# Kernel tuning notes

Hardware: AMD Instinct MI355X
Metric: run time of the kernel (lower is better)

Reference implementation:

```python
import jax, jax.numpy as jnp
import numpy as np

TAU = 18.0


def smooth_compose(X, M, tau=TAU):
    # Z[n,i,j] = smooth_min(X[n,i], M[i,j]) = -(1/tau) * log(exp(-tau*X) + exp(-tau*M))
    # Y[n,j]   = (1/tau) * logsumexp(tau * Z[n,:,j], axis over i)
    # tau*Z = -logaddexp(-tau*X, -tau*M)  (numerically stable, same math)
    tZ = -jnp.logaddexp(-tau * X[:, :, None], -tau * M[None, :, :])  # [n, d, d]
    return (1.0 / tau) * jax.nn.logsumexp(tZ, axis=1)  # [n, d]


def setup_inputs() -> dict:
    key = jax.random.key(0)
    k1, k2, k3, k4, k5 = jax.random.split(key, 5)
    n, p, d = 2048, 1024, 256
    S = jax.random.uniform(k1, (n, p), dtype=jnp.float32)
    T = jax.random.uniform(k2, (n, p), dtype=jnp.float32)
    # learned parameters (A0/M0/B0 defaults are 0.5-filled; use random values of similar scale)
    A = jax.random.uniform(k3, (p, d), dtype=jnp.float32)
    # rawM = logit(M0); random small logits -> M = sigmoid(rawM) near 0.5
    rawM = 0.5 * jax.random.normal(k4, (d, d), dtype=jnp.float32)
    B = jax.random.uniform(k5, (d, p), dtype=jnp.float32)
    return {"S": S, "T": T, "A": A, "rawM": rawM, "B": B}


def reference(S, T, A, rawM, B):
    M = jax.nn.sigmoid(rawM)            # [d, d]
    X_hat = S @ A                       # [n, d]
    Y_hat = T @ A                       # [n, d]
    X_box = jnp.clip(X_hat, 0.0, 1.0)
    Y_box = jnp.clip(Y_hat, 0.0, 1.0)
    Y_pred = smooth_compose(X_box, M, tau=TAU)  # [n, d]
    S_rec = X_hat @ B                   # [n, p]
    T_rec = Y_hat @ B                   # [n, p]
    T_pred = Y_pred @ B                 # [n, p]
    return (X_hat, Y_hat, X_box, Y_box, Y_pred, S_rec, T_rec, T_pred)
```

## Files before the change

kernel.cpp:

```cpp
#include <hip/hip_runtime.h>
#include <math.h>

constexpr int N = 2048;
constexpr int P = 1024;
constexpr int D = 256;
constexpr float TAU = 18.0f;

constexpr size_t OFF_XHAT  = 0;
constexpr size_t OFF_YHAT  = (size_t)N * D;
constexpr size_t OFF_XBOX  = 2 * (size_t)N * D;
constexpr size_t OFF_YBOX  = 3 * (size_t)N * D;
constexpr size_t OFF_YPRED = 4 * (size_t)N * D;
constexpr size_t OFF_SREC  = 5 * (size_t)N * D;

constexpr size_t WS_ATH = 0;
constexpr size_t WS_ATL = 524288;
constexpr size_t WS_BTH = 1048576;
constexpr size_t WS_BTL = 1572864;
constexpr size_t WS_V   = 2097152;
constexpr size_t WS_U   = 2359296;

typedef short bhalf8 __attribute__((ext_vector_type(8)));
typedef float f32x4  __attribute__((ext_vector_type(4)));

__device__ inline short f2bf(float f) {
  union { float f; unsigned u; } x; x.f = f;
  unsigned r = (x.u + 0x7FFFu + ((x.u >> 16) & 1u)) >> 16;
  return (short)r;
}
__device__ inline float bf2f(short h) {
  union { unsigned u; float f; } x; x.u = ((unsigned)(unsigned short)h) << 16;
  return x.f;
}

__global__ __launch_bounds__(256) void prep_v_kernel(
    const float* __restrict__ rawM, float* __restrict__ V) {
  const int idx = (blockIdx.x * 256 + threadIdx.x) * 4;
  float4 x = *(const float4*)(rawM + idx);
  float4 o;
  o.x = expf(-TAU / (1.0f + expf(-x.x)));
  o.y = expf(-TAU / (1.0f + expf(-x.y)));
  o.z = expf(-TAU / (1.0f + expf(-x.z)));
  o.w = expf(-TAU / (1.0f + expf(-x.w)));
  *(float4*)(V + idx) = o;
}

__global__ __launch_bounds__(256) void transpose_hilo_kernel(
    const float* __restrict__ src, short* __restrict__ dh,
    short* __restrict__ dl, int R, int C) {
  __shared__ __align__(16) float tile[32][36];
  const int t = threadIdx.x;
  const int r0 = blockIdx.x * 32, c0 = blockIdx.y * 32;
  {
    const int tr = t >> 3, tc4 = (t & 7) * 4;
    float4 x = *(const float4*)(src + (size_t)(r0 + tr) * C + c0 + tc4);
    *(float4*)&tile[tr][tc4] = x;
  }
  __syncthreads();
  {
    const int tc = t >> 3, tr4 = (t & 7) * 4;
    short4 h, l;
    float f0 = tile[tr4 + 0][tc];
    float f1 = tile[tr4 + 1][tc];
    float f2 = tile[tr4 + 2][tc];
    float f3 = tile[tr4 + 3][tc];
    h.x = f2bf(f0); l.x = f2bf(f0 - bf2f(h.x));
    h.y = f2bf(f1); l.y = f2bf(f1 - bf2f(h.y));
    h.z = f2bf(f2); l.z = f2bf(f2 - bf2f(h.z));
    h.w = f2bf(f3); l.w = f2bf(f3 - bf2f(h.w));
    *(short4*)(dh + (size_t)(c0 + tc) * R + r0 + tr4) = h;
    *(short4*)(dl + (size_t)(c0 + tc) * R + r0 + tr4) = l;
  }
}

__global__ __launch_bounds__(256) void gemm1_mfma(
    const float* __restrict__ S, const float* __restrict__ Tm,
    const short* __restrict__ Ath, const short* __restrict__ Atl,
    float* __restrict__ out, float* __restrict__ U) {
  __shared__ __align__(16) short As_h[64][40];
  __shared__ __align__(16) short As_l[64][40];
  __shared__ __align__(16) short Bs_h[64][40];
  __shared__ __align__(16) short Bs_l[64][40];

  const int t = threadIdx.x;
  const int m0 = blockIdx.x * 64, n0 = blockIdx.y * 64;

  const int arow = t >> 2;
  const int koct = (t & 3) * 8;
  const int grow = m0 + arow;
  const float* Lrow = (grow < N) ? (S + (size_t)grow * P)
                                 : (Tm + (size_t)(grow - N) * P);
  const short* Bh_row = Ath + (size_t)(n0 + arow) * P;
  const short* Bl_row = Atl + (size_t)(n0 + arow) * P;

  const int l = t & 63, w = t >> 6;
  const int wr = (w >> 1) * 32, wc = (w & 1) * 32;
  const int fr = l & 15;
  const int ko = (l >> 4) * 8;
  const int rq = (l >> 4) * 4;

  f32x4 acc[2][2];
#pragma unroll
  for (int i = 0; i < 2; ++i)
#pragma unroll
    for (int j = 0; j < 2; ++j) acc[i][j] = (f32x4){0.f, 0.f, 0.f, 0.f};

  float4 a0 = *(const float4*)(Lrow + koct);
  float4 a1 = *(const float4*)(Lrow + koct + 4);
  bhalf8 bh = *(const bhalf8*)(Bh_row + koct);
  bhalf8 bl = *(const bhalf8*)(Bl_row + koct);

  for (int ks = 0; ks < P / 32; ++ks) {
    __syncthreads();
    {
      float af[8] = {a0.x, a0.y, a0.z, a0.w, a1.x, a1.y, a1.z, a1.w};
      bhalf8 ah, al;
#pragma unroll
      for (int q = 0; q < 8; ++q) {
        short h = f2bf(af[q]);
        ah[q] = h;
        al[q] = f2bf(af[q] - bf2f(h));
      }
      *(bhalf8*)&As_h[arow][koct] = ah;
      *(bhalf8*)&As_l[arow][koct] = al;
      *(bhalf8*)&Bs_h[arow][koct] = bh;
      *(bhalf8*)&Bs_l[arow][koct] = bl;
    }
    __syncthreads();
    if (ks + 1 < P / 32) {
      const int kn = (ks + 1) * 32 + koct;
      a0 = *(const float4*)(Lrow + kn);
      a1 = *(const float4*)(Lrow + kn + 4);
      bh = *(const bhalf8*)(Bh_row + kn);
      bl = *(const bhalf8*)(Bl_row + kn);
    }
    bhalf8 avh[2], avl[2], bvh[2], bvl[2];
#pragma unroll
    for (int mi = 0; mi < 2; ++mi) {
      avh[mi] = *(const bhalf8*)&As_h[wr + mi * 16 + fr][ko];
      avl[mi] = *(const bhalf8*)&As_l[wr + mi * 16 + fr][ko];
      bvh[mi] = *(const bhalf8*)&Bs_h[wc + mi * 16 + fr][ko];
      bvl[mi] = *(const bhalf8*)&Bs_l[wc + mi * 16 + fr][ko];
    }
#pragma unroll
    for (int mi = 0; mi < 2; ++mi)
#pragma unroll
      for (int ni = 0; ni < 2; ++ni) {
        acc[mi][ni] = __builtin_amdgcn_mfma_f32_16x16x32_bf16(avh[mi], bvh[ni], acc[mi][ni], 0, 0, 0);
        acc[mi][ni] = __builtin_amdgcn_mfma_f32_16x16x32_bf16(avh[mi], bvl[ni], acc[mi][ni], 0, 0, 0);
        acc[mi][ni] = __builtin_amdgcn_mfma_f32_16x16x32_bf16(avl[mi], bvh[ni], acc[mi][ni], 0, 0, 0);
        acc[mi][ni] = __builtin_amdgcn_mfma_f32_16x16x32_bf16(avl[mi], bvl[ni], acc[mi][ni], 0, 0, 0);
      }
  }

#pragma unroll
  for (int mi = 0; mi < 2; ++mi)
#pragma unroll
    for (int ni = 0; ni < 2; ++ni) {
      const int col = n0 + wc + ni * 16 + fr;
#pragma unroll
      for (int r = 0; r < 4; ++r) {
        const int row = m0 + wr + mi * 16 + rq + r;
        const float v = acc[mi][ni][r];
        const float c = fminf(fmaxf(v, 0.0f), 1.0f);
        if (row < N) {
          out[OFF_XHAT + (size_t)row * D + col] = v;
          out[OFF_XBOX + (size_t)row * D + col] = c;
          U[(size_t)row * D + col] = expf(-TAU * c);
        } else {
          const size_t ry = (size_t)(row - N);
          out[OFF_YHAT + ry * D + col] = v;
          out[OFF_YBOX + ry * D + col] = c;
        }
      }
    }
}

__global__ __launch_bounds__(256) void smooth_kernel(
    const float* __restrict__ U, const float* __restrict__ V,
    float* __restrict__ ypred) {
  __shared__ float us[256][33];
  const int t = threadIdx.x;
  const int n0 = blockIdx.x * 32, j0 = blockIdx.y * 64;

  {
    const int sr = t & 31;
    const int si = (t >> 5) * 32;
    const float* up = U + (size_t)(n0 + sr) * D + si;
#pragma unroll
    for (int q = 0; q < 32; q += 4) {
      float4 x = *(const float4*)(up + q);
      us[si + q + 0][sr] = x.x;
      us[si + q + 1][sr] = x.y;
      us[si + q + 2][sr] = x.z;
      us[si + q + 3][sr] = x.w;
    }
  }
  __syncthreads();

  const int jg = (t & 15) * 4;
  const int nn = (t >> 4) * 2;
  const float* vp = V + j0 + jg;

  float acc[2][4] = {};
#pragma unroll 4
  for (int i = 0; i < D; ++i) {
    const float u0 = us[i][nn];
    const float u1 = us[i][nn + 1];
    float4 v4 = *(const float4*)(vp + (size_t)i * D);
    acc[0][0] += __builtin_amdgcn_rcpf(u0 + v4.x);
    acc[0][1] += __builtin_amdgcn_rcpf(u0 + v4.y);
    acc[0][2] += __builtin_amdgcn_rcpf(u0 + v4.z);
    acc[0][3] += __builtin_amdgcn_rcpf(u0 + v4.w);
    acc[1][0] += __builtin_amdgcn_rcpf(u1 + v4.x);
    acc[1][1] += __builtin_amdgcn_rcpf(u1 + v4.y);
    acc[1][2] += __builtin_amdgcn_rcpf(u1 + v4.z);
    acc[1][3] += __builtin_amdgcn_rcpf(u1 + v4.w);
  }
#pragma unroll
  for (int pI = 0; pI < 2; ++pI) {
    float4 o;
    o.x = (1.0f / TAU) * logf(acc[pI][0]);
    o.y = (1.0f / TAU) * logf(acc[pI][1]);
    o.z = (1.0f / TAU) * logf(acc[pI][2]);
    o.w = (1.0f / TAU) * logf(acc[pI][3]);
    *(float4*)(ypred + (size_t)(n0 + nn + pI) * D + j0 + jg) = o;
  }
}

__global__ __launch_bounds__(256) void gemm2_mfma(
    const float* __restrict__ dout, const short* __restrict__ Bth,
    const short* __restrict__ Btl, float* __restrict__ rec) {
  __shared__ __align__(16) short As_h[64][40];
  __shared__ __align__(16) short As_l[64][40];
  __shared__ __align__(16) short Bs_h[64][40];
  __shared__ __align__(16) short Bs_l[64][40];

  const int t = threadIdx.x;
  const int m0 = blockIdx.x * 64, n0 = blockIdx.y * 64;

  const int arow = t >> 2;
  const int koct = (t & 3) * 8;
  const int grow = m0 + arow;
  const float* Lrow = (grow < 2 * N)
                          ? (dout + (size_t)grow * D)
                          : (dout + OFF_YPRED + (size_t)(grow - 2 * N) * D);
  const short* Bh_row = Bth + (size_t)(n0 + arow) * D;
  const short* Bl_row = Btl + (size_t)(n0 + arow) * D;

  const int l = t & 63, w = t >> 6;
  const int wr = (w >> 1) * 32, wc = (w & 1) * 32;
  const int fr = l & 15;
  const int ko = (l >> 4) * 8;
  const int rq = (l >> 4) * 4;

  f32x4 acc[2][2];
#pragma unroll
  for (int i = 0; i < 2; ++i)
#pragma unroll
    for (int j = 0; j < 2; ++j) acc[i][j] = (f32x4){0.f, 0.f, 0.f, 0.f};

  float4 a0 = *(const float4*)(Lrow + koct);
  float4 a1 = *(const float4*)(Lrow + koct + 4);
  bhalf8 bh = *(const bhalf8*)(Bh_row + koct);
  bhalf8 bl = *(const bhalf8*)(Bl_row + koct);

  for (int ks = 0; ks < D / 32; ++ks) {
    __syncthreads();
    {
      float af[8] = {a0.x, a0.y, a0.z, a0.w, a1.x, a1.y, a1.z, a1.w};
      bhalf8 ah, al;
#pragma unroll
      for (int q = 0; q < 8; ++q) {
        short h = f2bf(af[q]);
        ah[q] = h;
        al[q] = f2bf(af[q] - bf2f(h));
      }
      *(bhalf8*)&As_h[arow][koct] = ah;
      *(bhalf8*)&As_l[arow][koct] = al;
      *(bhalf8*)&Bs_h[arow][koct] = bh;
      *(bhalf8*)&Bs_l[arow][koct] = bl;
    }
    __syncthreads();
    if (ks + 1 < D / 32) {
      const int kn = (ks + 1) * 32 + koct;
      a0 = *(const float4*)(Lrow + kn);
      a1 = *(const float4*)(Lrow + kn + 4);
      bh = *(const bhalf8*)(Bh_row + kn);
      bl = *(const bhalf8*)(Bl_row + kn);
    }
    bhalf8 avh[2], avl[2], bvh[2], bvl[2];
#pragma unroll
    for (int mi = 0; mi < 2; ++mi) {
      avh[mi] = *(const bhalf8*)&As_h[wr + mi * 16 + fr][ko];
      avl[mi] = *(const bhalf8*)&As_l[wr + mi * 16 + fr][ko];
      bvh[mi] = *(const bhalf8*)&Bs_h[wc + mi * 16 + fr][ko];
      bvl[mi] = *(const bhalf8*)&Bs_l[wc + mi * 16 + fr][ko];
    }
#pragma unroll
    for (int mi = 0; mi < 2; ++mi)
#pragma unroll
      for (int ni = 0; ni < 2; ++ni) {
        acc[mi][ni] = __builtin_amdgcn_mfma_f32_16x16x32_bf16(avh[mi], bvh[ni], acc[mi][ni], 0, 0, 0);
        acc[mi][ni] = __builtin_amdgcn_mfma_f32_16x16x32_bf16(avh[mi], bvl[ni], acc[mi][ni], 0, 0, 0);
        acc[mi][ni] = __builtin_amdgcn_mfma_f32_16x16x32_bf16(avl[mi], bvh[ni], acc[mi][ni], 0, 0, 0);
        acc[mi][ni] = __builtin_amdgcn_mfma_f32_16x16x32_bf16(avl[mi], bvl[ni], acc[mi][ni], 0, 0, 0);
      }
  }

#pragma unroll
  for (int mi = 0; mi < 2; ++mi)
#pragma unroll
    for (int ni = 0; ni < 2; ++ni) {
      const int col = n0 + wc + ni * 16 + fr;
#pragma unroll
      for (int r = 0; r < 4; ++r) {
        const int row = m0 + wr + mi * 16 + rq + r;
        rec[(size_t)row * P + col] = acc[mi][ni][r];
      }
    }
}

extern "C" void kernel_launch(void* const* d_in, const int* in_sizes, int n_in,
                              void* d_out, int out_size, void* d_ws,
                              size_t ws_size, hipStream_t stream) {
  const float* S    = (const float*)d_in[0];
  const float* T    = (const float*)d_in[1];
  const float* A    = (const float*)d_in[2];
  const float* rawM = (const float*)d_in[3];
  const float* B    = (const float*)d_in[4];
  float* out = (float*)d_out;
  char* ws = (char*)d_ws;

  short* Ath = (short*)(ws + WS_ATH);
  short* Atl = (short*)(ws + WS_ATL);
  short* Bth = (short*)(ws + WS_BTH);
  short* Btl = (short*)(ws + WS_BTL);
  float* V   = (float*)(ws + WS_V);
  float* U   = (float*)(ws + WS_U);

  prep_v_kernel<<<64, 256, 0, stream>>>(rawM, V);
  transpose_hilo_kernel<<<dim3(32, 8), 256, 0, stream>>>(A, Ath, Atl, P, D);
  transpose_hilo_kernel<<<dim3(8, 32), 256, 0, stream>>>(B, Bth, Btl, D, P);
  gemm1_mfma<<<dim3(64, 4), 256, 0, stream>>>(S, T, Ath, Atl, out, U);
  smooth_kernel<<<dim3(64, 4), 256, 0, stream>>>(U, V, out + OFF_YPRED);
  gemm2_mfma<<<dim3(96, 16), 256, 0, stream>>>(out, Bth, Btl, out + OFF_SREC);
}
```

Measured before the change: 158.7 us.

## Double-buffer GEMM tiles, drop lo*lo MFMA, pre-split GEMM2 operands to bf16

Both MFMA GEMMs move to 512-thread blocks with double-buffered LDS tiles and one barrier per k-step. The lo*lo bf16 correction product is dropped, removing a quarter of the MFMAs at a small precision cost. GEMM1 and the smooth kernel now write hi/lo bf16 splits of their outputs to workspace, so GEMM2 loads pre-split shorts instead of converting fp32 activations on each tile. The smooth kernel gets a smaller column tile to launch more blocks. The cost is extra workspace traffic for the split buffers.

```diff
diff --git a/kernel.cpp b/kernel.cpp
--- a/kernel.cpp
+++ b/kernel.cpp
@@ -19,6 +19,8 @@
 constexpr size_t WS_BTL = 1572864;
 constexpr size_t WS_V   = 2097152;
 constexpr size_t WS_U   = 2359296;
+constexpr size_t WS_LHH = 4456448;
+constexpr size_t WS_LHL = 7602176;
 
 typedef short bhalf8 __attribute__((ext_vector_type(8)));
 typedef float f32x4  __attribute__((ext_vector_type(4)));
@@ -73,115 +75,109 @@
   }
 }
 
-__global__ __launch_bounds__(256) void gemm1_mfma(
+__global__ __launch_bounds__(512) void gemm1_mfma(
     const float* __restrict__ S, const float* __restrict__ Tm,
     const short* __restrict__ Ath, const short* __restrict__ Atl,
-    float* __restrict__ out, float* __restrict__ U) {
-  __shared__ __align__(16) short As_h[64][40];
-  __shared__ __align__(16) short As_l[64][40];
-  __shared__ __align__(16) short Bs_h[64][40];
-  __shared__ __align__(16) short Bs_l[64][40];
-
-  const int t = threadIdx.x;
+    float* __restrict__ out, float* __restrict__ U,
+    short* __restrict__ LHh, short* __restrict__ LHl) {
+  __shared__ __align__(16) short As_h[2][64][40];
+  __shared__ __align__(16) short As_l[2][64][40];
+  __shared__ __align__(16) short Bs_h[2][64][40];
+  __shared__ __align__(16) short Bs_l[2][64][40];
+
+  const int t  = threadIdx.x;
   const int m0 = blockIdx.x * 64, n0 = blockIdx.y * 64;
 
-  const int arow = t >> 2;
-  const int koct = (t & 3) * 8;
-  const int grow = m0 + arow;
+  const int srow = t >> 3;
+  const int sk   = (t & 7) * 4;
+  const int grow = m0 + srow;
   const float* Lrow = (grow < N) ? (S + (size_t)grow * P)
                                  : (Tm + (size_t)(grow - N) * P);
-  const short* Bh_row = Ath + (size_t)(n0 + arow) * P;
-  const short* Bl_row = Atl + (size_t)(n0 + arow) * P;
+  const short* BhR = Ath + (size_t)(n0 + srow) * P;
+  const short* BlR = Atl + (size_t)(n0 + srow) * P;
 
   const int l = t & 63, w = t >> 6;
-  const int wr = (w >> 1) * 32, wc = (w & 1) * 32;
-  const int fr = l & 15;
-  const int ko = (l >> 4) * 8;
-  const int rq = (l >> 4) * 4;
-
-  f32x4 acc[2][2];
-#pragma unroll
-  for (int i = 0; i < 2; ++i)
-#pragma unroll
-    for (int j = 0; j < 2; ++j) acc[i][j] = (f32x4){0.f, 0.f, 0.f, 0.f};
-
-  float4 a0 = *(const float4*)(Lrow + koct);
-  float4 a1 = *(const float4*)(Lrow + koct + 4);
-  bhalf8 bh = *(const bhalf8*)(Bh_row + koct);
-  bhalf8 bl = *(const bhalf8*)(Bl_row + koct);
-
-  for (int ks = 0; ks < P / 32; ++ks) {
+  const int wr = (w & 3) * 16, wc = (w >> 2) * 32;
+  const int fr = l & 15, ko8 = (l >> 4) * 8, rq = (l >> 4) * 4;
+
+  f32x4 acc[2];
+  acc[0] = (f32x4){0.f, 0.f, 0.f, 0.f};
+  acc[1] = (f32x4){0.f, 0.f, 0.f, 0.f};
+
+  float4 pa  = *(const float4*)(Lrow + sk);
+  short4 pbh = *(const short4*)(BhR + sk);
+  short4 pbl = *(const short4*)(BlR + sk);
+
+#define STAGE1(buf)                                        \
+  do {                                                     \
+    short4 ah4, al4;                                       \
+    ah4.x = f2bf(pa.x); al4.x = f2bf(pa.x - bf2f(ah4.x));  \
+    ah4.y = f2bf(pa.y); al4.y = f2bf(pa.y - bf2f(ah4.y));  \
+    ah4.z = f2bf(pa.z); al4.z = f2bf(pa.z - bf2f(ah4.z));  \
+    ah4.w = f2bf(pa.w); al4.w = f2bf(pa.w - bf2f(ah4.w));  \
+    *(short4*)&As_h[buf][srow][sk] = ah4;                  \
+    *(short4*)&As_l[buf][srow][sk] = al4;                  \
+    *(short4*)&Bs_h[buf][srow][sk] = pbh;                  \
+    *(short4*)&Bs_l[buf][srow][sk] = pbl;                  \
+  } while (0)
+
+  STAGE1(0);
+
+  for (int ks = 0; ks < 32; ++ks) {
+    const int b = ks & 1;
+    if (ks < 31) {
+      const int kn = (ks + 1) * 32;
+      pa  = *(const float4*)(Lrow + kn + sk);
+      pbh = *(const short4*)(BhR + kn + sk);
+      pbl = *(const short4*)(BlR + kn + sk);
+    }
     __syncthreads();
-    {
-      float af[8] = {a0.x, a0.y, a0.z, a0.w, a1.x, a1.y, a1.z, a1.w};
-      bhalf8 ah, al;
-#pragma unroll
-      for (int q = 0; q < 8; ++q) {
-        short h = f2bf(af[q]);
-        ah[q] = h;
-        al[q] = f2bf(af[q] - bf2f(h));
+    bhalf8 ahv = *(const bhalf8*)&As_h[b][wr + fr][ko8];
+    bhalf8 alv = *(const bhalf8*)&As_l[b][wr + fr][ko8];
+#pragma unroll
+    for (int ni = 0; ni < 2; ++ni) {
+      bhalf8 bhv = *(const bhalf8*)&Bs_h[b][wc + ni * 16 + fr][ko8];
+      bhalf8 blv = *(const bhalf8*)&Bs_l[b][wc + ni * 16 + fr][ko8];
+      acc[ni] = __builtin_amdgcn_mfma_f32_16x16x32_bf16(ahv, bhv, acc[ni], 0, 0, 0);
+      acc[ni] = __builtin_amdgcn_mfma_f32_16x16x32_bf16(ahv, blv, acc[ni], 0, 0, 0);
+      acc[ni] = __builtin_amdgcn_mfma_f32_16x16x32_bf16(alv, bhv, acc[ni], 0, 0, 0);
+    }
+    if (ks < 31) STAGE1((ks + 1) & 1);
+  }
+#undef STAGE1
+
+#pragma unroll
+  for (int ni = 0; ni < 2; ++ni) {
+    const int col = n0 + wc + ni * 16 + fr;
+#pragma unroll
+    for (int r = 0; r < 4; ++r) {
+      const int row = m0 + wr + rq + r;
+      const float v = acc[ni][r];
+      const float c = fminf(fmaxf(v, 0.0f), 1.0f);
+      const short h  = f2bf(v);
+      const short lo = f2bf(v - bf2f(h));
+      LHh[(size_t)row * D + col] = h;
+      LHl[(size_t)row * D + col] = lo;
+      if (row < N) {
+        out[OFF_XHAT + (size_t)row * D + col] = v;
+        out[OFF_XBOX + (size_t)row * D + col] = c;
+        U[(size_t)row * D + col] = expf(-TAU * c);
+      } else {
+        const size_t ry = (size_t)(row - N);
+        out[OFF_YHAT + ry * D + col] = v;
+        out[OFF_YBOX + ry * D + col] = c;
       }
-      *(bhalf8*)&As_h[arow][koct] = ah;
-      *(bhalf8*)&As_l[arow][koct] = al;
-      *(bhalf8*)&Bs_h[arow][koct] = bh;
-      *(bhalf8*)&Bs_l[arow][koct] = bl;
-    }
-    __syncthreads();
-    if (ks + 1 < P / 32) {
-      const int kn = (ks + 1) * 32 + koct;
-      a0 = *(const float4*)(Lrow + kn);
-      a1 = *(const float4*)(Lrow + kn + 4);
-      bh = *(const bhalf8*)(Bh_row + kn);
-      bl = *(const bhalf8*)(Bl_row + kn);
-    }
-    bhalf8 avh[2], avl[2], bvh[2], bvl[2];
-#pragma unroll
-    for (int mi = 0; mi < 2; ++mi) {
-      avh[mi] = *(const bhalf8*)&As_h[wr + mi * 16 + fr][ko];
-      avl[mi] = *(const bhalf8*)&As_l[wr + mi * 16 + fr][ko];
-      bvh[mi] = *(const bhalf8*)&Bs_h[wc + mi * 16 + fr][ko];
-      bvl[mi] = *(const bhalf8*)&Bs_l[wc + mi * 16 + fr][ko];
-    }
-#pragma unroll
-    for (int mi = 0; mi < 2; ++mi)
-#pragma unroll
-      for (int ni = 0; ni < 2; ++ni) {
-        acc[mi][ni] = __builtin_amdgcn_mfma_f32_16x16x32_bf16(avh[mi], bvh[ni], acc[mi][ni], 0, 0, 0);
-        acc[mi][ni] = __builtin_amdgcn_mfma_f32_16x16x32_bf16(avh[mi], bvl[ni], acc[mi][ni], 0, 0, 0);
-        acc[mi][ni] = __builtin_amdgcn_mfma_f32_16x16x32_bf16(avl[mi], bvh[ni], acc[mi][ni], 0, 0, 0);
-        acc[mi][ni] = __builtin_amdgcn_mfma_f32_16x16x32_bf16(avl[mi], bvl[ni], acc[mi][ni], 0, 0, 0);
-      }
-  }
-
-#pragma unroll
-  for (int mi = 0; mi < 2; ++mi)
-#pragma unroll
-    for (int ni = 0; ni < 2; ++ni) {
-      const int col = n0 + wc + ni * 16 + fr;
-#pragma unroll
-      for (int r = 0; r < 4; ++r) {
-        const int row = m0 + wr + mi * 16 + rq + r;
-        const float v = acc[mi][ni][r];
-        const float c = fminf(fmaxf(v, 0.0f), 1.0f);
-        if (row < N) {
-          out[OFF_XHAT + (size_t)row * D + col] = v;
-          out[OFF_XBOX + (size_t)row * D + col] = c;
-          U[(size_t)row * D + col] = expf(-TAU * c);
-        } else {
-          const size_t ry = (size_t)(row - N);
-          out[OFF_YHAT + ry * D + col] = v;
-          out[OFF_YBOX + ry * D + col] = c;
-        }
-      }
-    }
+    }
+  }
 }
 
 __global__ __launch_bounds__(256) void smooth_kernel(
     const float* __restrict__ U, const float* __restrict__ V,
-    float* __restrict__ ypred) {
-  __shared__ float us[256][33];
+    float* __restrict__ ypred, short* __restrict__ LHh,
+    short* __restrict__ LHl) {
+  __shared__ float us[256][34];
   const int t = threadIdx.x;
-  const int n0 = blockIdx.x * 32, j0 = blockIdx.y * 64;
+  const int n0 = blockIdx.x * 32, j0 = blockIdx.y * 32;
 
   {
     const int sr = t & 31;
@@ -198,127 +194,113 @@
   }
   __syncthreads();
 
-  const int jg = (t & 15) * 4;
+  const int jg = (t & 15) * 2;
   const int nn = (t >> 4) * 2;
   const float* vp = V + j0 + jg;
 
-  float acc[2][4] = {};
-#pragma unroll 4
+  float acc00 = 0.f, acc01 = 0.f, acc10 = 0.f, acc11 = 0.f;
+#pragma unroll 8
   for (int i = 0; i < D; ++i) {
-    const float u0 = us[i][nn];
-    const float u1 = us[i][nn + 1];
-    float4 v4 = *(const float4*)(vp + (size_t)i * D);
-    acc[0][0] += __builtin_amdgcn_rcpf(u0 + v4.x);
-    acc[0][1] += __builtin_amdgcn_rcpf(u0 + v4.y);
-    acc[0][2] += __builtin_amdgcn_rcpf(u0 + v4.z);
-    acc[0][3] += __builtin_amdgcn_rcpf(u0 + v4.w);
-    acc[1][0] += __builtin_amdgcn_rcpf(u1 + v4.x);
-    acc[1][1] += __builtin_amdgcn_rcpf(u1 + v4.y);
-    acc[1][2] += __builtin_amdgcn_rcpf(u1 + v4.z);
-    acc[1][3] += __builtin_amdgcn_rcpf(u1 + v4.w);
-  }
+    float2 u2 = *(const float2*)&us[i][nn];
+    float2 v2 = *(const float2*)(vp + (size_t)i * D);
+    acc00 += __builtin_amdgcn_rcpf(u2.x + v2.x);
+    acc01 += __builtin_amdgcn_rcpf(u2.x + v2.y);
+    acc10 += __builtin_amdgcn_rcpf(u2.y + v2.x);
+    acc11 += __builtin_amdgcn_rcpf(u2.y + v2.y);
+  }
+
+  float a[2][2] = {{acc00, acc01}, {acc10, acc11}};
 #pragma unroll
   for (int pI = 0; pI < 2; ++pI) {
-    float4 o;
-    o.x = (1.0f / TAU) * logf(acc[pI][0]);
-    o.y = (1.0f / TAU) * logf(acc[pI][1]);
-    o.z = (1.0f / TAU) * logf(acc[pI][2]);
-    o.w = (1.0f / TAU) * logf(acc[pI][3]);
-    *(float4*)(ypred + (size_t)(n0 + nn + pI) * D + j0 + jg) = o;
-  }
-}
-
-__global__ __launch_bounds__(256) void gemm2_mfma(
-    const float* __restrict__ dout, const short* __restrict__ Bth,
-    const short* __restrict__ Btl, float* __restrict__ rec) {
-  __shared__ __align__(16) short As_h[64][40];
-  __shared__ __align__(16) short As_l[64][40];
-  __shared__ __align__(16) short Bs_h[64][40];
-  __shared__ __align__(16) short Bs_l[64][40];
-
-  const int t = threadIdx.x;
+    const int row = n0 + nn + pI;
+    float2 o;
+    o.x = (1.0f / TAU) * logf(a[pI][0]);
+    o.y = (1.0f / TAU) * logf(a[pI][1]);
+    *(float2*)(ypred + (size_t)row * D + j0 + jg) = o;
+    short2 h2, l2;
+    h2.x = f2bf(o.x); l2.x = f2bf(o.x - bf2f(h2.x));
+    h2.y = f2bf(o.y); l2.y = f2bf(o.y - bf2f(h2.y));
+    const size_t lrow = (size_t)(2 * N + row) * D + j0 + jg;
+    *(short2*)(LHh + lrow) = h2;
+    *(short2*)(LHl + lrow) = l2;
+  }
+}
+
+__global__ __launch_bounds__(512) void gemm2_mfma(
+    const short* __restrict__ LHh, const short* __restrict__ LHl,
+    const short* __restrict__ Bth, const short* __restrict__ Btl,
+    float* __restrict__ rec) {
+  __shared__ __align__(16) short As_h[2][64][40];
+  __shared__ __align__(16) short As_l[2][64][40];
+  __shared__ __align__(16) short Bs_h[2][64][40];
+  __shared__ __align__(16) short Bs_l[2][64][40];
+
+  const int t  = threadIdx.x;
   const int m0 = blockIdx.x * 64, n0 = blockIdx.y * 64;
 
-  const int arow = t >> 2;
-  const int koct = (t & 3) * 8;
-  const int grow = m0 + arow;
-  const float* Lrow = (grow < 2 * N)
-                          ? (dout + (size_t)grow * D)
-                          : (dout + OFF_YPRED + (size_t)(grow - 2 * N) * D);
-  const short* Bh_row = Bth + (size_t)(n0 + arow) * D;
-  const short* Bl_row = Btl + (size_t)(n0 + arow) * D;
+  const int srow = t >> 3;
+  const int sk   = (t & 7) * 4;
+  const short* AhR = LHh + (size_t)(m0 + srow) * D;
+  const short* AlR = LHl + (size_t)(m0 + srow) * D;
+  const short* BhR = Bth + (size_t)(n0 + srow) * D;
+  const short* BlR = Btl + (size_t)(n0 + srow) * D;
 
   const int l = t & 63, w = t >> 6;
-  const int wr = (w >> 1) * 32, wc = (w & 1) * 32;
-  const int fr = l & 15;
-  const int ko = (l >> 4) * 8;
-  const int rq = (l >> 4) * 4;
-
-  f32x4 acc[2][2];
-#pragma unroll
-  for (int i = 0; i < 2; ++i)
-#pragma unroll
-    for (int j = 0; j < 2; ++j) acc[i][j] = (f32x4){0.f, 0.f, 0.f, 0.f};
-
-  float4 a0 = *(const float4*)(Lrow + koct);
-  float4 a1 = *(const float4*)(Lrow + koct + 4);
-  bhalf8 bh = *(const bhalf8*)(Bh_row + koct);
-  bhalf8 bl = *(const bhalf8*)(Bl_row + koct);
-
-  for (int ks = 0; ks < D / 32; ++ks) {
+  const int wr = (w & 3) * 16, wc = (w >> 2) * 32;
+  const int fr = l & 15, ko8 = (l >> 4) * 8, rq = (l >> 4) * 4;
+
+  f32x4 acc[2];
+  acc[0] = (f32x4){0.f, 0.f, 0.f, 0.f};
+  acc[1] = (f32x4){0.f, 0.f, 0.f, 0.f};
+
+  short4 pah = *(const short4*)(AhR + sk);
+  short4 pal = *(const short4*)(AlR + sk);
+  short4 pbh = *(const short4*)(BhR + sk);
+  short4 pbl = *(const short4*)(BlR + sk);
+
+#define STAGE2(buf)                            \
+  do {                                         \
+    *(short4*)&As_h[buf][srow][sk] = pah;      \
+    *(short4*)&As_l[buf][srow][sk] = pal;      \
+    *(short4*)&Bs_h[buf][srow][sk] = pbh;      \
+    *(short4*)&Bs_l[buf][srow][sk] = pbl;      \
+  } while (0)
+
+  STAGE2(0);
+
+  for (int ks = 0; ks < 8; ++ks) {
+    const int b = ks & 1;
+    if (ks < 7) {
+      const int kn = (ks + 1) * 32;
+      pah = *(const short4*)(AhR + kn + sk);
+      pal = *(const short4*)(AlR + kn + sk);
+      pbh = *(const short4*)(BhR + kn + sk);
+      pbl = *(const short4*)(BlR + kn + sk);
+    }
     __syncthreads();
-    {
-      float af[8] = {a0.x, a0.y, a0.z, a0.w, a1.x, a1.y, a1.z, a1.w};
-      bhalf8 ah, al;
-#pragma unroll
-      for (int q = 0; q < 8; ++q) {
-        short h = f2bf(af[q]);
-        ah[q] = h;
-        al[q] = f2bf(af[q] - bf2f(h));
-      }
-      *(bhalf8*)&As_h[arow][koct] = ah;
-      *(bhalf8*)&As_l[arow][koct] = al;
-      *(bhalf8*)&Bs_h[arow][koct] = bh;
-      *(bhalf8*)&Bs_l[arow][koct] = bl;
-    }
-    __syncthreads();
-    if (ks + 1 < D / 32) {
-      const int kn = (ks + 1) * 32 + koct;
-      a0 = *(const float4*)(Lrow + kn);
-      a1 = *(const float4*)(Lrow + kn + 4);
-      bh = *(const bhalf8*)(Bh_row + kn);
-      bl = *(const bhalf8*)(Bl_row + kn);
-    }
-    bhalf8 avh[2], avl[2], bvh[2], bvl[2];
-#pragma unroll
-    for (int mi = 0; mi < 2; ++mi) {
-      avh[mi] = *(const bhalf8*)&As_h[wr + mi * 16 + fr][ko];
-      avl[mi] = *(const bhalf8*)&As_l[wr + mi * 16 + fr][ko];
-      bvh[mi] = *(const bhalf8*)&Bs_h[wc + mi * 16 + fr][ko];
-      bvl[mi] = *(const bhalf8*)&Bs_l[wc + mi * 16 + fr][ko];
-    }
-#pragma unroll
-    for (int mi = 0; mi < 2; ++mi)
-#pragma unroll
-      for (int ni = 0; ni < 2; ++ni) {
-        acc[mi][ni] = __builtin_amdgcn_mfma_f32_16x16x32_bf16(avh[mi], bvh[ni], acc[mi][ni], 0, 0, 0);
-        acc[mi][ni] = __builtin_amdgcn_mfma_f32_16x16x32_bf16(avh[mi], bvl[ni], acc[mi][ni], 0, 0, 0);
-        acc[mi][ni] = __builtin_amdgcn_mfma_f32_16x16x32_bf16(avl[mi], bvh[ni], acc[mi][ni], 0, 0, 0);
-        acc[mi][ni] = __builtin_amdgcn_mfma_f32_16x16x32_bf16(avl[mi], bvl[ni], acc[mi][ni], 0, 0, 0);
-      }
-  }
-
-#pragma unroll
-  for (int mi = 0; mi < 2; ++mi)
+    bhalf8 ahv = *(const bhalf8*)&As_h[b][wr + fr][ko8];
+    bhalf8 alv = *(const bhalf8*)&As_l[b][wr + fr][ko8];
 #pragma unroll
     for (int ni = 0; ni < 2; ++ni) {
-      const int col = n0 + wc + ni * 16 + fr;
-#pragma unroll
-      for (int r = 0; r < 4; ++r) {
-        const int row = m0 + wr + mi * 16 + rq + r;
-        rec[(size_t)row * P + col] = acc[mi][ni][r];
-      }
-    }
+      bhalf8 bhv = *(const bhalf8*)&Bs_h[b][wc + ni * 16 + fr][ko8];
+      bhalf8 blv = *(const bhalf8*)&Bs_l[b][wc + ni * 16 + fr][ko8];
+      acc[ni] = __builtin_amdgcn_mfma_f32_16x16x32_bf16(ahv, bhv, acc[ni], 0, 0, 0);
+      acc[ni] = __builtin_amdgcn_mfma_f32_16x16x32_bf16(ahv, blv, acc[ni], 0, 0, 0);
+      acc[ni] = __builtin_amdgcn_mfma_f32_16x16x32_bf16(alv, bhv, acc[ni], 0, 0, 0);
+    }
+    if (ks < 7) STAGE2((ks + 1) & 1);
+  }
+#undef STAGE2
+
+#pragma unroll
+  for (int ni = 0; ni < 2; ++ni) {
+    const int col = n0 + wc + ni * 16 + fr;
+#pragma unroll
+    for (int r = 0; r < 4; ++r) {
+      const int row = m0 + wr + rq + r;
+      rec[(size_t)row * P + col] = acc[ni][r];
+    }
+  }
 }
 
 extern "C" void kernel_launch(void* const* d_in, const int* in_sizes, int n_in,
@@ -338,11 +320,13 @@
   short* Btl = (short*)(ws + WS_BTL);
   float* V   = (float*)(ws + WS_V);
   float* U   = (float*)(ws + WS_U);
+  short* LHh = (short*)(ws + WS_LHH);
+  short* LHl = (short*)(ws + WS_LHL);
 
   prep_v_kernel<<<64, 256, 0, stream>>>(rawM, V);
   transpose_hilo_kernel<<<dim3(32, 8), 256, 0, stream>>>(A, Ath, Atl, P, D);
   transpose_hilo_kernel<<<dim3(8, 32), 256, 0, stream>>>(B, Bth, Btl, D, P);
-  gemm1_mfma<<<dim3(64, 4), 256, 0, stream>>>(S, T, Ath, Atl, out, U);
-  smooth_kernel<<<dim3(64, 4), 256, 0, stream>>>(U, V, out + OFF_YPRED);
-  gemm2_mfma<<<dim3(96, 16), 256, 0, stream>>>(out, Bth, Btl, out + OFF_SREC);
-}
+  gemm1_mfma<<<dim3(64, 4), 512, 0, stream>>>(S, T, Ath, Atl, out, U, LHh, LHl);
+  smooth_kernel<<<dim3(64, 8), 256, 0, stream>>>(U, V, out + OFF_YPRED, LHh, LHl);
+  gemm2_mfma<<<dim3(96, 16), 512, 0, stream>>>(LHh, LHl, Bth, Btl, out + OFF_SREC);
+}
```

After: 138.7 us. 12.6% less time.
